# Kernel optimization log

Measured on AMD Instinct MI355X. Metric: run time of the kernel, lower is better.

The kernel has to match this reference:

```python
import jax, jax.numpy as jnp
import numpy as np

B, N, D = 16, 2048, 128  # batch, nodes, embedding_dim

def setup_inputs() -> dict:
    key = jax.random.key(0)
    ks = jax.random.split(key, 12)
    def dense(kw, kb, din, dout):
        # keras Dense default glorot_uniform weight, zeros bias (use small random bias for generality)
        lim = np.sqrt(6.0 / (din + dout))
        W = jax.random.uniform(kw, (din, dout), minval=-lim, maxval=lim, dtype=jnp.float32)
        b = jax.random.normal(kb, (dout,), dtype=jnp.float32) * 0.01
        return W, b
    Wq, bq = dense(ks[0], ks[1], D, D)
    Wk, bk = dense(ks[2], ks[3], D, D)
    Wv, bv = dense(ks[4], ks[5], D, D)
    Wo, bo = dense(ks[6], ks[7], D, D)
    query_ = jax.random.normal(ks[8], (B, N, D), dtype=jnp.float32)
    key_ = jax.random.normal(ks[9], (B, N, D), dtype=jnp.float32)
    mask = jax.random.randint(ks[10], (B, N + 1, N + 1), 0, 2).astype(bool)
    return {"query_": query_, "key_": key_, "mask": mask,
            "Wq": Wq, "bq": bq, "Wk": Wk, "bk": bk,
            "Wv": Wv, "bv": bv, "Wo": Wo, "bo": bo}

def reference(query_, key_, mask, Wq, bq, Wk, bk, Wv, bv, Wo, bo):
    q = query_ @ Wq + bq                       # [B,N,D]
    k = key_ @ Wk + bk                         # [B,N,D]
    comp = jnp.einsum('bqd,bkd->bqk', q, k)    # [B,N,N]
    comp = comp / jnp.sqrt(jnp.asarray(k.shape[-1], jnp.float32))
    m = mask[:, 1:, 1:]                        # [B,N,N]
    comp = jnp.where(m, -jnp.inf, comp)
    attn = jax.nn.softmax(comp, axis=-1)
    attn = jnp.where(jnp.isnan(attn), 0.0, attn)  # fully-masked rows -> 0
    # NOTE: faithful to source: value projection applied to the PROJECTED key
    v = k @ Wv + bv                            # [B,N,D]
    out = jnp.einsum('bqk,bkd->bqd', attn, v)
    return out @ Wo + bo
```

## Files before the change

kernel.cpp:

```cpp
#include <hip/hip_runtime.h>

#define SB 16
#define SN 2048
#define SD 128
#define NM 2049
#define SZ (SB*SN*SD)

typedef __bf16 bf16x8 __attribute__((ext_vector_type(8)));
typedef float f32x4 __attribute__((ext_vector_type(4)));
typedef unsigned long long u64;

__device__ __forceinline__ unsigned short f2b(float f){
  union { float f; unsigned int u; } v; v.f = f;
  unsigned int r = v.u + 0x7fffu + ((v.u >> 16) & 1u);
  return (unsigned short)(r >> 16);
}

__device__ __forceinline__ void async16(const void* g, void* l){
  __builtin_amdgcn_global_load_lds(
      (__attribute__((address_space(1))) void*)(g),
      (__attribute__((address_space(3))) void*)(l), 16, 0, 0);
}

__global__ __launch_bounds__(256) void prep_w_kernel(
    const float* __restrict__ Wq, const float* __restrict__ Wk,
    const float* __restrict__ Wv, const float* __restrict__ Wo,
    unsigned short* __restrict__ out)
{
  int widx = blockIdx.x >> 4;
  int kg   = blockIdx.x & 15;
  const float* W = (widx==0)?Wq:(widx==1)?Wk:(widx==2)?Wv:Wo;
  unsigned short* O = out + widx*16384;
  int t = threadIdx.x;
  int k = kg*8 + (t>>5);
  int n = (t&31)*4;
  float4 v = *reinterpret_cast<const float4*>(W + k*SD + n);
  O[(n+0)*SD + k] = f2b(v.x);
  O[(n+1)*SD + k] = f2b(v.y);
  O[(n+2)*SD + k] = f2b(v.z);
  O[(n+3)*SD + k] = f2b(v.w);
}

__global__ __launch_bounds__(256) void prep_wkv_kernel(
    const float* __restrict__ Wk, const float* __restrict__ Wv,
    const float* __restrict__ bk, const float* __restrict__ bv,
    unsigned short* __restrict__ WkvT, float* __restrict__ bkv)
{
  int t = threadIdx.x;
  int k = blockIdx.x*8 + (t>>5);
  int n0 = (t&31)*4;
  float ax=0.f, ay=0.f, az=0.f, aw=0.f;
  for (int m=0;m<SD;m++){
    float wk = Wk[k*SD+m];
    float4 wv = *reinterpret_cast<const float4*>(Wv + m*SD + n0);
    ax += wk*wv.x; ay += wk*wv.y; az += wk*wv.z; aw += wk*wv.w;
  }
  WkvT[(n0+0)*SD + k] = f2b(ax);
  WkvT[(n0+1)*SD + k] = f2b(ay);
  WkvT[(n0+2)*SD + k] = f2b(az);
  WkvT[(n0+3)*SD + k] = f2b(aw);
  if (blockIdx.x==0 && t < SD){
    float a = 0.f;
    for (int m=0;m<SD;m++) a += bk[m]*Wv[m*SD + t];
    bkv[t] = a + bv[t];
  }
}

__global__ __launch_bounds__(256,4) void qkv_pack_kernel(
    const float* __restrict__ query, const float* __restrict__ key,
    const int* __restrict__ mask,
    const unsigned short* __restrict__ wts,
    const float* __restrict__ bq, const float* __restrict__ bk,
    const float* __restrict__ bkv,
    unsigned short* __restrict__ qb, unsigned short* __restrict__ kb,
    unsigned short* __restrict__ vt, u64* __restrict__ pmask)
{
  __shared__ unsigned short vT[128*72];

  int tid=threadIdx.x;
  int w=tid>>6, ln=tid&63, g=ln>>4, lm=ln&15;
  int bi = blockIdx.x;

  if (bi >= 1024){
    int pid = bi - 1024;
    for (int rr=0; rr<4; rr++){
      int row = pid*16 + w*4 + rr;
      int b = row >> 11, qr = row & 2047;
      const int* src = mask + (size_t)b*NM*NM + (size_t)(1+qr)*NM + 1;
      u64* dst = pmask + (size_t)row*32;
      for (int i=0;i<32;i++){
        int m = __builtin_nontemporal_load(src + i*64 + ln);
        u64 bal = __ballot(m != 0);
        if (ln == 0) dst[i] = bal;
      }
    }
    return;
  }

  int id = bi >> 1;
  int b = id >> 5, nt = id & 31;
  size_t rowbase = (size_t)b*SN + nt*64 + w*16;

  if ((bi & 1) == 0){
    const unsigned short* WkT  = wts + 16384;
    const unsigned short* WkvT = wts + 32768;
    const float* xr = key + (rowbase + lm)*SD;
    bf16x8 af[4];
    for (int ks=0;ks<4;ks++){
      float4 x0 = *reinterpret_cast<const float4*>(xr + ks*32 + g*8);
      float4 x1 = *reinterpret_cast<const float4*>(xr + ks*32 + g*8 + 4);
      union { bf16x8 v; unsigned short s[8]; } u;
      u.s[0]=f2b(x0.x); u.s[1]=f2b(x0.y); u.s[2]=f2b(x0.z); u.s[3]=f2b(x0.w);
      u.s[4]=f2b(x1.x); u.s[5]=f2b(x1.y); u.s[6]=f2b(x1.z); u.s[7]=f2b(x1.w);
      af[ks]=u.v;
    }
    for (int d=0; d<8; d++){
      f32x4 acc = {0.f,0.f,0.f,0.f};
      for (int ks=0;ks<4;ks++){
        bf16x8 wf = *reinterpret_cast<const bf16x8*>(WkT + (d*16+lm)*SD + ks*32 + g*8);
        acc = __builtin_amdgcn_mfma_f32_16x16x32_bf16(af[ks], wf, acc, 0,0,0);
      }
      float bb = bk[d*16+lm];
      for (int r=0;r<4;r++)
        kb[(rowbase + 4*g + r)*SD + d*16 + lm] = f2b(acc[r]+bb);
    }
    for (int d=0; d<8; d++){
      f32x4 acc = {0.f,0.f,0.f,0.f};
      for (int ks=0;ks<4;ks++){
        bf16x8 wf = *reinterpret_cast<const bf16x8*>(WkvT + (d*16+lm)*SD + ks*32 + g*8);
        acc = __builtin_amdgcn_mfma_f32_16x16x32_bf16(wf, af[ks], acc, 0,0,0);
      }
      float4 bb = *reinterpret_cast<const float4*>(bkv + d*16 + 4*g);
      vT[(d*16 + 4*g + 0)*72 + w*16 + lm] = f2b(acc[0]+bb.x);
      vT[(d*16 + 4*g + 1)*72 + w*16 + lm] = f2b(acc[1]+bb.y);
      vT[(d*16 + 4*g + 2)*72 + w*16 + lm] = f2b(acc[2]+bb.z);
      vT[(d*16 + 4*g + 3)*72 + w*16 + lm] = f2b(acc[3]+bb.w);
    }
    __syncthreads();
    int d = tid>>1, half = tid&1;
    const uint4* src4 = reinterpret_cast<const uint4*>(&vT[d*72 + half*32]);
    uint4* dst4 = reinterpret_cast<uint4*>(vt + (size_t)b*SD*SN + (size_t)d*SN + nt*64 + half*32);
    dst4[0]=src4[0]; dst4[1]=src4[1]; dst4[2]=src4[2]; dst4[3]=src4[3];
  } else {
    const unsigned short* WqT = wts;
    const float sc = 0.08838834764831845f;
    const float* xr = query + (rowbase + lm)*SD;
    bf16x8 af[4];
    for (int ks=0;ks<4;ks++){
      float4 x0 = *reinterpret_cast<const float4*>(xr + ks*32 + g*8);
      float4 x1 = *reinterpret_cast<const float4*>(xr + ks*32 + g*8 + 4);
      union { bf16x8 v; unsigned short s[8]; } u;
      u.s[0]=f2b(x0.x); u.s[1]=f2b(x0.y); u.s[2]=f2b(x0.z); u.s[3]=f2b(x0.w);
      u.s[4]=f2b(x1.x); u.s[5]=f2b(x1.y); u.s[6]=f2b(x1.z); u.s[7]=f2b(x1.w);
      af[ks]=u.v;
    }
    for (int d=0; d<8; d++){
      f32x4 acc = {0.f,0.f,0.f,0.f};
      for (int ks=0;ks<4;ks++){
        bf16x8 wf = *reinterpret_cast<const bf16x8*>(WqT + (d*16+lm)*SD + ks*32 + g*8);
        acc = __builtin_amdgcn_mfma_f32_16x16x32_bf16(af[ks], wf, acc, 0,0,0);
      }
      float bb = bq[d*16+lm];
      for (int r=0;r<4;r++)
        qb[(rowbase + 4*g + r)*SD + d*16 + lm] = f2b((acc[r]+bb)*sc);
    }
  }
}

__global__ __launch_bounds__(256,4) void flash_kernel(
    const unsigned short* __restrict__ qb, const unsigned short* __restrict__ kb,
    const unsigned short* __restrict__ vt, const u64* __restrict__ pmask,
    const unsigned short* __restrict__ WoT, const float* __restrict__ bo,
    float* __restrict__ out)
{
  __shared__ unsigned short bufK[2][64*128];
  __shared__ unsigned short bufV[2][128*64];
  __shared__ unsigned short ldsP[4*16*72];

  int tid=threadIdx.x;
  int w=tid>>6, ln=tid&63, g=ln>>4, lm=ln&15;
  int xcd   = blockIdx.x & 7;
  int inner = blockIdx.x >> 3;
  int b  = xcd*2 + (inner>>5);
  int qt = inner & 31;
  int q0 = qt*64;

  const unsigned short* Qb = qb + (size_t)b*SN*SD;
  const unsigned short* Kb = kb + (size_t)b*SN*SD;
  const unsigned short* Vb = vt + (size_t)b*SD*SN;

  auto issueK = [&](int k0, int bi){
    const char* gbase = (const char*)Kb + (size_t)k0*256;
    for (int c=0;c<4;c++){
      int p = c*256 + tid;
      int row = p>>4, lc = (p&15) ^ (row&15);
      async16(gbase + (size_t)row*256 + lc*16, (char*)bufK[bi] + p*16);
    }
  };
  auto issueV = [&](int k0, int bi){
    const char* gbase = (const char*)Vb + (size_t)k0*2;
    for (int c=0;c<4;c++){
      int p = c*256 + tid;
      int row = p>>3, lc = (p&7) ^ (row&7);
      async16(gbase + (size_t)row*4096 + lc*16, (char*)bufV[bi] + p*16);
    }
  };

  issueK(0,0); issueV(0,0);

  bf16x8 qf[4];
  {
    const unsigned short* qr = Qb + (size_t)(q0 + w*16 + lm)*SD;
    for (int ks=0;ks<4;ks++)
      qf[ks] = *reinterpret_cast<const bf16x8*>(qr + ks*32 + g*8);
  }

  const u64* pmb = pmask + ((size_t)(b*2048 + q0 + w*16 + 4*g))*32;
  u64 mb[4];
#pragma unroll
  for (int r=0;r<4;r++) mb[r] = pmb[r*32];

  float mrow[4], lrow[4], al[4];
  f32x4 acc[8];
  for (int r=0;r<4;r++){ mrow[r]=-INFINITY; lrow[r]=0.f; }
  for (int d=0;d<8;d++){ f32x4 z={0.f,0.f,0.f,0.f}; acc[d]=z; }
  unsigned short* pw = &ldsP[w*16*72];

  for (int kt=0; kt<32; kt++){
    __syncthreads();
    int cur = kt&1;
    if (kt<31){ issueK((kt+1)*64, cur^1); issueV((kt+1)*64, cur^1); }

    f32x4 s[4];
    __builtin_amdgcn_s_setprio(1);
    for (int ct=0;ct<4;ct++){
      f32x4 z = {0.f,0.f,0.f,0.f};
      for (int ks=0;ks<4;ks++){
        bf16x8 kf = *reinterpret_cast<const bf16x8*>(
            &bufK[cur][(ct*16+lm)*128 + (((ks*4+g)^lm))*8]);
        z = __builtin_amdgcn_mfma_f32_16x16x32_bf16(qf[ks], kf, z, 0,0,0);
      }
      s[ct]=z;
    }
    __builtin_amdgcn_s_setprio(0);

#pragma unroll
    for (int ct=0;ct<4;ct++){
      unsigned wlo, sh;
#pragma unroll
      for (int r=0;r<4;r++){
        if (ct < 2){ wlo = (unsigned)mb[r];        sh = ct*16 + lm; }
        else       { wlo = (unsigned)(mb[r]>>32);  sh = (ct-2)*16 + lm; }
        if ((wlo >> sh) & 1u) s[ct][r] = -INFINITY;
      }
    }
    if (kt<31){
#pragma unroll
      for (int r=0;r<4;r++) mb[r] = pmb[r*32 + kt + 1];
    }

    for (int r=0;r<4;r++){
      float v = fmaxf(fmaxf(s[0][r],s[1][r]), fmaxf(s[2][r],s[3][r]));
      v = fmaxf(v, __shfl_xor(v,1,16));
      v = fmaxf(v, __shfl_xor(v,2,16));
      v = fmaxf(v, __shfl_xor(v,4,16));
      v = fmaxf(v, __shfl_xor(v,8,16));
      float mn = fmaxf(mrow[r], v);
      bool dead = (mn == -INFINITY);
      float a = dead ? 1.f : __expf(mrow[r]-mn);
      float rsum = 0.f;
      for (int ct=0;ct<4;ct++){
        float p = dead ? 0.f : __expf(s[ct][r]-mn);
        s[ct][r]=p; rsum += p;
      }
      rsum += __shfl_xor(rsum,1,16);
      rsum += __shfl_xor(rsum,2,16);
      rsum += __shfl_xor(rsum,4,16);
      rsum += __shfl_xor(rsum,8,16);
      lrow[r] = lrow[r]*a + rsum;
      mrow[r] = mn;
      al[r] = a;
    }
    for (int d=0;d<8;d++)
      for (int r=0;r<4;r++)
        acc[d][r] *= al[r];

    for (int ct=0;ct<4;ct++){
      int col = ct*16+lm;
      for (int r=0;r<4;r++)
        pw[(4*g+r)*72 + col] = f2b(s[ct][r]);
    }
    bf16x8 pa0 = *reinterpret_cast<const bf16x8*>(&pw[lm*72 + g*8]);
    bf16x8 pa1 = *reinterpret_cast<const bf16x8*>(&pw[lm*72 + 32 + g*8]);

    __builtin_amdgcn_s_setprio(1);
    for (int d=0;d<8;d++){
      bf16x8 v0 = *reinterpret_cast<const bf16x8*>(
          &bufV[cur][(d*16+lm)*64 + ((g^(lm&7)))*8]);
      acc[d] = __builtin_amdgcn_mfma_f32_16x16x32_bf16(pa0, v0, acc[d], 0,0,0);
      bf16x8 v1 = *reinterpret_cast<const bf16x8*>(
          &bufV[cur][(d*16+lm)*64 + (((4+g)^(lm&7)))*8]);
      acc[d] = __builtin_amdgcn_mfma_f32_16x16x32_bf16(pa1, v1, acc[d], 0,0,0);
    }
    __builtin_amdgcn_s_setprio(0);
  }

  __syncthreads();
  float inv[4];
  for (int r=0;r<4;r++) inv[r] = (lrow[r] > 0.f) ? (1.f/lrow[r]) : 0.f;
  unsigned short* strip = &bufK[0][0] + w*2176;
  for (int d=0;d<8;d++)
    for (int r=0;r<4;r++)
      strip[(4*g+r)*136 + d*16 + lm] = f2b(acc[d][r]*inv[r]);
  bf16x8 oa[4];
  for (int ks=0;ks<4;ks++)
    oa[ks] = *reinterpret_cast<const bf16x8*>(&strip[lm*136 + ks*32 + g*8]);
  float* Ob = out + ((size_t)b*SN + q0 + w*16)*SD;
  for (int dc=0; dc<8; dc++){
    f32x4 o = {0.f,0.f,0.f,0.f};
    for (int ks=0;ks<4;ks++){
      bf16x8 wf = *reinterpret_cast<const bf16x8*>(WoT + (dc*16+lm)*SD + ks*32 + g*8);
      o = __builtin_amdgcn_mfma_f32_16x16x32_bf16(oa[ks], wf, o, 0,0,0);
    }
    float bb = bo[dc*16+lm];
    for (int r=0;r<4;r++)
      __builtin_nontemporal_store(o[r]+bb, &Ob[(size_t)(4*g+r)*SD + dc*16 + lm]);
  }
}

extern "C" void kernel_launch(void* const* d_in, const int* in_sizes, int n_in,
                              void* d_out, int out_size, void* d_ws, size_t ws_size,
                              hipStream_t stream)
{
  const float* query = (const float*)d_in[0];
  const float* key   = (const float*)d_in[1];
  const int*   mask  = (const int*)d_in[2];
  const float* Wq = (const float*)d_in[3];
  const float* bq = (const float*)d_in[4];
  const float* Wk = (const float*)d_in[5];
  const float* bk = (const float*)d_in[6];
  const float* Wv = (const float*)d_in[7];
  const float* bv = (const float*)d_in[8];
  const float* Wo = (const float*)d_in[9];
  const float* bo = (const float*)d_in[10];
  float* out = (float*)d_out;

  unsigned short* qb = (unsigned short*)d_ws;
  unsigned short* kb = qb + SZ;
  unsigned short* vt = kb + SZ;
  unsigned short* wts = vt + SZ;
  float* bkv = (float*)(wts + 65536);
  u64* pmask = (u64*)(bkv + 128);

  prep_w_kernel  <<<64,256,0,stream>>>(Wq,Wk,Wv,Wo,wts);
  prep_wkv_kernel<<<16,256,0,stream>>>(Wk,Wv,bk,bv, wts+32768, bkv);
  qkv_pack_kernel<<<3072,256,0,stream>>>(query, key, mask, wts, bq, bk, bkv,
                                         qb, kb, vt, pmask);
  flash_kernel   <<<512,256,0,stream>>>(qb, kb, vt, pmask, wts+49152, bo, out);
}
```

Baseline: 601.5 us.

## Switch mask to byte-per-element layout and stage Q/K stores through LDS

Replaces the ballot-packed 64-bit bitmask with a byte-per-element mask that the flash kernel reads directly per lane. Mask packing blocks now each handle 32 rows with 4-wide loads, so the grid shrinks. Q and K projection results are staged in shared memory and written out as coalesced 16-byte stores instead of scattered 2-byte stores. The byte mask is 8x larger, which adds global traffic in both the pack kernel and the flash kernel's per-tile mask loads.

```diff
diff --git a/kernel.cpp b/kernel.cpp
--- a/kernel.cpp
+++ b/kernel.cpp
@@ -8,7 +8,6 @@
 
 typedef __bf16 bf16x8 __attribute__((ext_vector_type(8)));
 typedef float f32x4 __attribute__((ext_vector_type(4)));
-typedef unsigned long long u64;
 
 __device__ __forceinline__ unsigned short f2b(float f){
   union { float f; unsigned int u; } v; v.f = f;
@@ -66,16 +65,17 @@
   }
 }
 
-__global__ __launch_bounds__(256,4) void qkv_pack_kernel(
+__global__ __launch_bounds__(256,4) void qkv_kernel(
     const float* __restrict__ query, const float* __restrict__ key,
     const int* __restrict__ mask,
     const unsigned short* __restrict__ wts,
     const float* __restrict__ bq, const float* __restrict__ bk,
     const float* __restrict__ bkv,
     unsigned short* __restrict__ qb, unsigned short* __restrict__ kb,
-    unsigned short* __restrict__ vt, u64* __restrict__ pmask)
+    unsigned short* __restrict__ vt, unsigned char* __restrict__ pmask8)
 {
   __shared__ unsigned short vT[128*72];
+  __shared__ unsigned short kq[4][16*136];
 
   int tid=threadIdx.x;
   int w=tid>>6, ln=tid&63, g=ln>>4, lm=ln&15;
@@ -83,15 +83,18 @@
 
   if (bi >= 1024){
     int pid = bi - 1024;
-    for (int rr=0; rr<4; rr++){
-      int row = pid*16 + w*4 + rr;
+    for (int rr=0; rr<8; rr++){
+      int row = pid*32 + w*8 + rr;
       int b = row >> 11, qr = row & 2047;
       const int* src = mask + (size_t)b*NM*NM + (size_t)(1+qr)*NM + 1;
-      u64* dst = pmask + (size_t)row*32;
-      for (int i=0;i<32;i++){
-        int m = __builtin_nontemporal_load(src + i*64 + ln);
-        u64 bal = __ballot(m != 0);
-        if (ln == 0) dst[i] = bal;
+      unsigned char* dst = pmask8 + (size_t)row*2048;
+      for (int j=0;j<8;j++){
+        int c = j*256 + ln*4;
+        unsigned int pv =  (src[c+0]?1u:0u)
+                        | ((src[c+1]?1u:0u)<<8)
+                        | ((src[c+2]?1u:0u)<<16)
+                        | ((src[c+3]?1u:0u)<<24);
+        *reinterpret_cast<unsigned int*>(dst + c) = pv;
       }
     }
     return;
@@ -100,6 +103,8 @@
   int id = bi >> 1;
   int b = id >> 5, nt = id & 31;
   size_t rowbase = (size_t)b*SN + nt*64 + w*16;
+  unsigned short* st = &kq[w][0];
+  int srow = ln>>2, sqtr = ln&3;
 
   if ((bi & 1) == 0){
     const unsigned short* WkT  = wts + 16384;
@@ -122,7 +127,13 @@
       }
       float bb = bk[d*16+lm];
       for (int r=0;r<4;r++)
-        kb[(rowbase + 4*g + r)*SD + d*16 + lm] = f2b(acc[r]+bb);
+        st[(4*g+r)*136 + d*16 + lm] = f2b(acc[r]+bb);
+    }
+    asm volatile("" ::: "memory");
+    {
+      const uint4* s4 = reinterpret_cast<const uint4*>(&st[srow*136 + sqtr*32]);
+      uint4* d4 = reinterpret_cast<uint4*>(kb + (rowbase + srow)*SD + sqtr*32);
+      d4[0]=s4[0]; d4[1]=s4[1]; d4[2]=s4[2]; d4[3]=s4[3];
     }
     for (int d=0; d<8; d++){
       f32x4 acc = {0.f,0.f,0.f,0.f};
@@ -162,14 +173,20 @@
       }
       float bb = bq[d*16+lm];
       for (int r=0;r<4;r++)
-        qb[(rowbase + 4*g + r)*SD + d*16 + lm] = f2b((acc[r]+bb)*sc);
+        st[(4*g+r)*136 + d*16 + lm] = f2b((acc[r]+bb)*sc);
+    }
+    asm volatile("" ::: "memory");
+    {
+      const uint4* s4 = reinterpret_cast<const uint4*>(&st[srow*136 + sqtr*32]);
+      uint4* d4 = reinterpret_cast<uint4*>(qb + (rowbase + srow)*SD + sqtr*32);
+      d4[0]=s4[0]; d4[1]=s4[1]; d4[2]=s4[2]; d4[3]=s4[3];
     }
   }
 }
 
 __global__ __launch_bounds__(256,4) void flash_kernel(
     const unsigned short* __restrict__ qb, const unsigned short* __restrict__ kb,
-    const unsigned short* __restrict__ vt, const u64* __restrict__ pmask,
+    const unsigned short* __restrict__ vt, const unsigned char* __restrict__ pmask8,
     const unsigned short* __restrict__ WoT, const float* __restrict__ bo,
     float* __restrict__ out)
 {
@@ -215,10 +232,11 @@
       qf[ks] = *reinterpret_cast<const bf16x8*>(qr + ks*32 + g*8);
   }
 
-  const u64* pmb = pmask + ((size_t)(b*2048 + q0 + w*16 + 4*g))*32;
-  u64 mb[4];
-#pragma unroll
-  for (int r=0;r<4;r++) mb[r] = pmb[r*32];
+  const unsigned char* pmb = pmask8 + ((size_t)(b*2048 + q0 + w*16 + 4*g))*2048 + lm;
+  int mreg[16];
+  for (int ct=0;ct<4;ct++)
+    for (int r=0;r<4;r++)
+      mreg[ct*4+r] = pmb[r*2048 + ct*16];
 
   float mrow[4], lrow[4], al[4];
   f32x4 acc[8];
@@ -244,19 +262,14 @@
     }
     __builtin_amdgcn_s_setprio(0);
 
-#pragma unroll
-    for (int ct=0;ct<4;ct++){
-      unsigned wlo, sh;
-#pragma unroll
-      for (int r=0;r<4;r++){
-        if (ct < 2){ wlo = (unsigned)mb[r];        sh = ct*16 + lm; }
-        else       { wlo = (unsigned)(mb[r]>>32);  sh = (ct-2)*16 + lm; }
-        if ((wlo >> sh) & 1u) s[ct][r] = -INFINITY;
-      }
-    }
+    for (int ct=0;ct<4;ct++)
+      for (int r=0;r<4;r++)
+        s[ct][r] = mreg[ct*4+r] ? -INFINITY : s[ct][r];
     if (kt<31){
-#pragma unroll
-      for (int r=0;r<4;r++) mb[r] = pmb[r*32 + kt + 1];
+      const unsigned char* mp = pmb + (kt+1)*64;
+      for (int ct=0;ct<4;ct++)
+        for (int r=0;r<4;r++)
+          mreg[ct*4+r] = mp[r*2048 + ct*16];
     }
 
     for (int r=0;r<4;r++){
@@ -290,8 +303,10 @@
       for (int r=0;r<4;r++)
         pw[(4*g+r)*72 + col] = f2b(s[ct][r]);
     }
+    asm volatile("" ::: "memory");
     bf16x8 pa0 = *reinterpret_cast<const bf16x8*>(&pw[lm*72 + g*8]);
     bf16x8 pa1 = *reinterpret_cast<const bf16x8*>(&pw[lm*72 + 32 + g*8]);
+    asm volatile("" ::: "memory");
 
     __builtin_amdgcn_s_setprio(1);
     for (int d=0;d<8;d++){
@@ -312,9 +327,11 @@
   for (int d=0;d<8;d++)
     for (int r=0;r<4;r++)
       strip[(4*g+r)*136 + d*16 + lm] = f2b(acc[d][r]*inv[r]);
+  asm volatile("" ::: "memory");
   bf16x8 oa[4];
   for (int ks=0;ks<4;ks++)
     oa[ks] = *reinterpret_cast<const bf16x8*>(&strip[lm*136 + ks*32 + g*8]);
+  asm volatile("" ::: "memory");
   float* Ob = out + ((size_t)b*SN + q0 + w*16)*SD;
   for (int dc=0; dc<8; dc++){
     f32x4 o = {0.f,0.f,0.f,0.f};
@@ -350,11 +367,11 @@
   unsigned short* vt = kb + SZ;
   unsigned short* wts = vt + SZ;
   float* bkv = (float*)(wts + 65536);
-  u64* pmask = (u64*)(bkv + 128);
+  unsigned char* pmask8 = (unsigned char*)(bkv + 128);
 
   prep_w_kernel  <<<64,256,0,stream>>>(Wq,Wk,Wv,Wo,wts);
   prep_wkv_kernel<<<16,256,0,stream>>>(Wk,Wv,bk,bv, wts+32768, bkv);
-  qkv_pack_kernel<<<3072,256,0,stream>>>(query, key, mask, wts, bq, bk, bkv,
-                                         qb, kb, vt, pmask);
-  flash_kernel   <<<512,256,0,stream>>>(qb, kb, vt, pmask, wts+49152, bo, out);
-}
+  qkv_kernel     <<<2048,256,0,stream>>>(query, key, mask, wts, bq, bk, bkv,
+                                         qb, kb, vt, pmask8);
+  flash_kernel   <<<512,256,0,stream>>>(qb, kb, vt, pmask8, wts+49152, bo, out);
+}
```

Result: faster. 537.3 us (-10.7%).
